# Kernel optimization log

Hardware: AMD Instinct MI355X
Metric: run time of the kernel (lower is better)

The kernel has to match this reference:

```python
import jax, jax.numpy as jnp
import numpy as np

NBINS = (128, 64, 32)   # knots per stacked transform
N_GENES = 5000
N_ELEM = 4_000_000


def _split_parameters(unnormalized):
    # mirror of QuadraticSplineStack._split_parameters: [heights(n), widths(n-1)] per transform
    splits = []
    for n in NBINS:
        splits += [n, n - 1]
    parts = jnp.split(unnormalized, np.cumsum(splits)[:-1].tolist(), axis=-1)
    return list(zip(parts[0::2], parts[1::2]))


def _bin_search(table, gix, x):
    # vectorized per-element binary search: searchsorted(table[gix], x, side='right') - 1,
    # clamped to valid bin range [0, K-2]. table: [G, K] sorted; gix, x: [N].
    K = table.shape[-1]
    lo = jnp.zeros(x.shape, jnp.int32)
    hi = jnp.full(x.shape, K, jnp.int32)
    for _ in range(int(np.ceil(np.log2(K + 1)))):
        mid = jnp.clip((lo + hi) // 2, 0, K - 1)
        pred = table[gix, mid] <= x
        lo = jnp.where(pred, mid + 1, lo)
        hi = jnp.where(pred, hi, mid)
    return jnp.clip(lo - 1, 0, K - 2)


def _quadratic_spline_forward(x, gix, unnorm_heights, unnorm_widths):
    # per-gene tables
    widths = jax.nn.softmax(unnorm_widths, axis=-1)                      # [G, n-1]
    locs = jnp.cumsum(widths, axis=-1)
    locs = jnp.pad(locs.at[:, -1].set(1.0), ((0, 0), (1, 0)))            # [G, n] bin_locations
    eh = jnp.exp(unnorm_heights)                                         # [G, n]
    area = jnp.sum(0.5 * (eh[:, :-1] + eh[:, 1:]) * widths, axis=-1, keepdims=True)
    heights = eh / area                                                  # pdf knot heights, integrates to 1
    cdf = jnp.cumsum(0.5 * (heights[:, :-1] + heights[:, 1:]) * widths, axis=-1)
    left_cdf = jnp.pad(cdf.at[:, -1].set(1.0), ((0, 0), (1, 0)))         # [G, n] bin_left_cdf

    # locate bin per element, then gather scalar coefficients
    b = _bin_search(locs, gix, x)                                        # [N] in [0, n-2]
    w = widths[gix, b]
    lh = heights[gix, b]
    rh = heights[gix, b + 1]
    bl = locs[gix, b]
    lc = left_cdf[gix, b]

    alpha = (x - bl) / w
    out = (0.5 * (rh - lh) * w) * alpha * alpha + (lh * w) * alpha + lc
    out = jnp.clip(out, 0.0, 1.0)
    logabsdet = jnp.log(alpha * (rh - lh) + lh)
    return out, logabsdet


def setup_inputs() -> dict:
    key = jax.random.key(0)
    k1, k2, k3 = jax.random.split(key, 3)
    x = jax.random.uniform(k1, (N_ELEM,), dtype=jnp.float32, minval=1e-4, maxval=1.0 - 1e-4)
    local_gene_ix = jax.random.randint(k2, (N_ELEM,), 0, N_GENES)
    total = sum(n + (n - 1) for n in NBINS)  # 445
    unnormalized = jax.random.normal(k3, (N_GENES, total), dtype=jnp.float32) * 0.1
    return {"x": x, "local_gene_ix": local_gene_ix, "unnormalized": unnormalized}


def reference(x, local_gene_ix, unnormalized):
    gix = local_gene_ix.astype(jnp.int32)
    outputs = x
    logabsdet = jnp.zeros_like(x)
    for uh, uw in _split_parameters(unnormalized):
        outputs, lad = _quadratic_spline_forward(outputs, gix, uh, uw)
        logabsdet = logabsdet + lad
    return outputs, logabsdet
```

## Files before the change

kernel.cpp:

```cpp
#include <hip/hip_runtime.h>
#include <hip/hip_bf16.h>
#include <hip/hip_fp16.h>

#define N_GENES_MAX 5000
#define PARAMS_PER_GENE 445

#define KNOTS_PER_GENE 224

__device__ uint2 g_knots[(size_t)N_GENES_MAX * KNOTS_PER_GENE];

static __device__ __forceinline__ unsigned short f2h(float f) {
    union { __half h; unsigned short u; } c;
    c.h = __float2half_rn(f);
    return c.u;
}
static __device__ __forceinline__ float h2f(unsigned short u) {
    union { unsigned short u; __half h; } c;
    c.u = u;
    return __half2float(c.h);
}

__global__ void build_knots(const float* __restrict__ params) {
    const int g = blockIdx.x;
    const int t = blockIdx.y;
    const int ns[3]   = {128, 64, 32};
    const int poff[3] = {0, 255, 382};
    const int koff[3] = {0, 128, 192};

    const int n = ns[t];
    const int m = n - 1;
    const float* ph = params + (size_t)g * PARAMS_PER_GENE + poff[t];
    const float* pw = ph + n;

    __shared__ float s_scan[128];
    __shared__ float s_h[129];
    __shared__ float s_red[128];
    __shared__ float s_loc[128];
    __shared__ float s_cdf[128];

    const int tid = threadIdx.x;

    float uw = (tid < m) ? pw[tid] : -1e30f;
    s_red[tid] = uw;
    __syncthreads();
    for (int s = 64; s > 0; s >>= 1) {
        if (tid < s) s_red[tid] = fmaxf(s_red[tid], s_red[tid + s]);
        __syncthreads();
    }
    const float mx = s_red[0];
    __syncthreads();
    float e = (tid < m) ? expf(uw - mx) : 0.0f;

    s_scan[tid] = e;
    __syncthreads();
    #pragma unroll
    for (int off = 1; off < 128; off <<= 1) {
        float v = (tid >= off) ? s_scan[tid - off] : 0.0f;
        __syncthreads();
        s_scan[tid] += v;
        __syncthreads();
    }
    const float S = s_scan[m - 1];
    const float invS = 1.0f / S;
    const float w_i = e * invS;
    if (tid == 0) s_loc[0] = 0.0f;
    if (tid < m) s_loc[tid + 1] = (tid == m - 1) ? 1.0f : s_scan[tid] * invS;
    __syncthreads();

    float uh = (tid < n) ? ph[tid] : 0.0f;
    float eh = (tid < n) ? expf(uh) : 0.0f;
    s_h[tid] = eh;
    if (tid == 0) s_h[128] = 0.0f;
    __syncthreads();
    float term = (tid < m) ? 0.5f * (s_h[tid] + s_h[tid + 1]) * w_i : 0.0f;
    s_red[tid] = term;
    __syncthreads();
    for (int s = 64; s > 0; s >>= 1) {
        if (tid < s) s_red[tid] += s_red[tid + s];
        __syncthreads();
    }
    const float area = s_red[0];
    __syncthreads();
    const float inv_area = 1.0f / area;
    const float hgt = eh * inv_area;

    float d = term * inv_area;
    s_scan[tid] = d;
    __syncthreads();
    #pragma unroll
    for (int off = 1; off < 128; off <<= 1) {
        float v = (tid >= off) ? s_scan[tid - off] : 0.0f;
        __syncthreads();
        s_scan[tid] += v;
        __syncthreads();
    }
    if (tid == 0) s_cdf[0] = 0.0f;
    if (tid < m) s_cdf[tid + 1] = (tid == m - 1) ? 1.0f : s_scan[tid];
    __syncthreads();

    if (tid < n) {
        uint2 kt;
        kt.x = __float_as_uint(s_loc[tid]);
        kt.y = ((unsigned)f2h(s_cdf[tid]) << 16) | (unsigned)f2h(hgt);
        g_knots[(size_t)g * KNOTS_PER_GENE + koff[t] + tid] = kt;
    }
}

template <int K>
__device__ __forceinline__ void spline_stage(const uint2* __restrict__ kn,
                                             float& x, float& lad) {
    int b = (int)(x * (float)(K - 1));
    b = (b < 0) ? 0 : ((b > K - 2) ? K - 2 : b);
    uint2 k0 = kn[b];
    uint2 k1 = kn[b + 1];
    float l0 = __uint_as_float(k0.x);
    float l1 = __uint_as_float(k1.x);
    while (b > 0 && l0 > x) {
        --b;
        k1 = k0; l1 = l0;
        k0 = kn[b]; l0 = __uint_as_float(k0.x);
    }
    while (b < K - 2 && l1 <= x) {
        ++b;
        k0 = k1; l0 = l1;
        k1 = kn[b + 1]; l1 = __uint_as_float(k1.x);
    }
    const float lh = h2f((unsigned short)(k0.y & 0xffffu));
    const float lc = h2f((unsigned short)(k0.y >> 16));
    const float rh = h2f((unsigned short)(k1.y & 0xffffu));
    const float w  = l1 - l0;
    const float alpha = (x - l0) / w;
    float o = (0.5f * (rh - lh) * w) * alpha * alpha + (lh * w) * alpha + lc;
    o = fminf(fmaxf(o, 0.0f), 1.0f);
    lad += __logf(alpha * (rh - lh) + lh);
    x = o;
}

__global__ void spline_eval_gather(const float* __restrict__ x_in,
                                   const int* __restrict__ gix,
                                   float* __restrict__ out, int N) {
    const int i = blockIdx.x * blockDim.x + threadIdx.x;
    if (i >= N) return;
    float x = x_in[i];
    const uint2* tab = g_knots + (size_t)gix[i] * KNOTS_PER_GENE;
    float lad = 0.0f;
    spline_stage<128>(tab, x, lad);
    spline_stage<64>(tab + 128, x, lad);
    spline_stage<32>(tab + 192, x, lad);
    out[i] = x;
    out[N + i] = lad;
}

extern "C" void kernel_launch(void* const* d_in, const int* in_sizes, int n_in,
                              void* d_out, int out_size, void* d_ws, size_t ws_size,
                              hipStream_t stream) {
    const float* x      = (const float*)d_in[0];
    const int*   gix    = (const int*)d_in[1];
    const float* params = (const float*)d_in[2];
    float* out = (float*)d_out;

    const int N = in_sizes[0];
    const int G = in_sizes[2] / PARAMS_PER_GENE;

    build_knots<<<dim3(G, 3), 128, 0, stream>>>(params);

    const int block = 256;
    spline_eval_gather<<<(N + block - 1) / block, block, 0, stream>>>(x, gix, out, N);
}
```

Baseline: 212.2 us.

## Store per-bin float4 records and process two elements per thread

Knot tables become per-bin float4 records holding left and right location, left CDF, and packed fp16 left and right heights. Each bin lookup is then a single 16-byte gather instead of two 8-byte gathers. The eval kernel also handles two elements per thread with vectorized float2/int2 loads and stores, giving more independent gathers in flight. The trade-off is a larger table footprint (16B per bin versus 8B per knot), which puts more pressure on L2/MALL for random per-gene access.

```diff
diff --git a/kernel.cpp b/kernel.cpp
--- a/kernel.cpp
+++ b/kernel.cpp
@@ -5,18 +5,18 @@
 #define N_GENES_MAX 5000
 #define PARAMS_PER_GENE 445
 
-#define KNOTS_PER_GENE 224
+__device__ float4 g_rec0[(size_t)N_GENES_MAX * 127];
+__device__ float4 g_rec1[(size_t)N_GENES_MAX * 63];
+__device__ float4 g_rec2[(size_t)N_GENES_MAX * 31];
 
-__device__ uint2 g_knots[(size_t)N_GENES_MAX * KNOTS_PER_GENE];
-
-static __device__ __forceinline__ unsigned short f2h(float f) {
+static __device__ __forceinline__ unsigned f2h(float f) {
     union { __half h; unsigned short u; } c;
     c.h = __float2half_rn(f);
-    return c.u;
+    return (unsigned)c.u;
 }
-static __device__ __forceinline__ float h2f(unsigned short u) {
+static __device__ __forceinline__ float h2f(unsigned u) {
     union { unsigned short u; __half h; } c;
-    c.u = u;
+    c.u = (unsigned short)u;
     return __half2float(c.h);
 }
 
@@ -25,7 +25,6 @@
     const int t = blockIdx.y;
     const int ns[3]   = {128, 64, 32};
     const int poff[3] = {0, 255, 382};
-    const int koff[3] = {0, 128, 192};
 
     const int n = ns[t];
     const int m = n - 1;
@@ -37,6 +36,7 @@
     __shared__ float s_red[128];
     __shared__ float s_loc[128];
     __shared__ float s_cdf[128];
+    __shared__ float s_hgt[128];
 
     const int tid = threadIdx.x;
 
@@ -62,9 +62,9 @@
     }
     const float S = s_scan[m - 1];
     const float invS = 1.0f / S;
-    const float w_i = e * invS;
     if (tid == 0) s_loc[0] = 0.0f;
     if (tid < m) s_loc[tid + 1] = (tid == m - 1) ? 1.0f : s_scan[tid] * invS;
+    const float w_i = e * invS;
     __syncthreads();
 
     float uh = (tid < n) ? ph[tid] : 0.0f;
@@ -82,7 +82,7 @@
     const float area = s_red[0];
     __syncthreads();
     const float inv_area = 1.0f / area;
-    const float hgt = eh * inv_area;
+    if (tid < n) s_hgt[tid] = eh * inv_area;
 
     float d = term * inv_area;
     s_scan[tid] = d;
@@ -98,57 +98,64 @@
     if (tid < m) s_cdf[tid + 1] = (tid == m - 1) ? 1.0f : s_scan[tid];
     __syncthreads();
 
-    if (tid < n) {
-        uint2 kt;
-        kt.x = __float_as_uint(s_loc[tid]);
-        kt.y = ((unsigned)f2h(s_cdf[tid]) << 16) | (unsigned)f2h(hgt);
-        g_knots[(size_t)g * KNOTS_PER_GENE + koff[t] + tid] = kt;
+    if (tid < m) {
+        float4 r;
+        r.x = s_loc[tid];
+        r.y = s_loc[tid + 1];
+        r.z = s_cdf[tid];
+        r.w = __uint_as_float((f2h(s_hgt[tid + 1]) << 16) | f2h(s_hgt[tid]));
+        if (t == 0)      g_rec0[(size_t)g * 127 + tid] = r;
+        else if (t == 1) g_rec1[(size_t)g * 63 + tid] = r;
+        else             g_rec2[(size_t)g * 31 + tid] = r;
     }
 }
 
 template <int K>
-__device__ __forceinline__ void spline_stage(const uint2* __restrict__ kn,
+static __device__ __forceinline__ void stage(const float4* __restrict__ rec,
                                              float& x, float& lad) {
     int b = (int)(x * (float)(K - 1));
     b = (b < 0) ? 0 : ((b > K - 2) ? K - 2 : b);
-    uint2 k0 = kn[b];
-    uint2 k1 = kn[b + 1];
-    float l0 = __uint_as_float(k0.x);
-    float l1 = __uint_as_float(k1.x);
-    while (b > 0 && l0 > x) {
-        --b;
-        k1 = k0; l1 = l0;
-        k0 = kn[b]; l0 = __uint_as_float(k0.x);
-    }
-    while (b < K - 2 && l1 <= x) {
-        ++b;
-        k0 = k1; l0 = l1;
-        k1 = kn[b + 1]; l1 = __uint_as_float(k1.x);
-    }
-    const float lh = h2f((unsigned short)(k0.y & 0xffffu));
-    const float lc = h2f((unsigned short)(k0.y >> 16));
-    const float rh = h2f((unsigned short)(k1.y & 0xffffu));
-    const float w  = l1 - l0;
-    const float alpha = (x - l0) / w;
-    float o = (0.5f * (rh - lh) * w) * alpha * alpha + (lh * w) * alpha + lc;
+    float4 r = rec[b];
+    while (b > 0 && r.x > x) { --b; r = rec[b]; }
+    while (b < K - 2 && r.y <= x) { ++b; r = rec[b]; }
+    const float w = r.y - r.x;
+    const float alpha = (x - r.x) / w;
+    const unsigned hp = __float_as_uint(r.w);
+    const float lh = h2f(hp & 0xffffu);
+    const float rh = h2f(hp >> 16);
+    float o = (0.5f * (rh - lh) * w) * alpha * alpha + (lh * w) * alpha + r.z;
     o = fminf(fmaxf(o, 0.0f), 1.0f);
     lad += __logf(alpha * (rh - lh) + lh);
     x = o;
 }
 
-__global__ void spline_eval_gather(const float* __restrict__ x_in,
-                                   const int* __restrict__ gix,
-                                   float* __restrict__ out, int N) {
+static __device__ __forceinline__ void eval_one(float& x, int g, float& lad) {
+    stage<128>(g_rec0 + (size_t)g * 127, x, lad);
+    stage<64> (g_rec1 + (size_t)g * 63,  x, lad);
+    stage<32> (g_rec2 + (size_t)g * 31,  x, lad);
+}
+
+__global__ void spline_eval(const float* __restrict__ x_in,
+                            const int* __restrict__ gix,
+                            float* __restrict__ out, int N) {
     const int i = blockIdx.x * blockDim.x + threadIdx.x;
-    if (i >= N) return;
-    float x = x_in[i];
-    const uint2* tab = g_knots + (size_t)gix[i] * KNOTS_PER_GENE;
-    float lad = 0.0f;
-    spline_stage<128>(tab, x, lad);
-    spline_stage<64>(tab + 128, x, lad);
-    spline_stage<32>(tab + 192, x, lad);
-    out[i] = x;
-    out[N + i] = lad;
+    const int i2 = i * 2;
+    if (i2 + 1 < N) {
+        const float2 xv = *(const float2*)(x_in + i2);
+        const int2   gv = *(const int2*)(gix + i2);
+        float x0 = xv.x, x1 = xv.y;
+        float l0 = 0.0f, l1 = 0.0f;
+        eval_one(x0, gv.x, l0);
+        eval_one(x1, gv.y, l1);
+        *(float2*)(out + i2)     = make_float2(x0, x1);
+        *(float2*)(out + N + i2) = make_float2(l0, l1);
+    } else if (i2 < N) {
+        float x0 = x_in[i2];
+        float l0 = 0.0f;
+        eval_one(x0, gix[i2], l0);
+        out[i2] = x0;
+        out[N + i2] = l0;
+    }
 }
 
 extern "C" void kernel_launch(void* const* d_in, const int* in_sizes, int n_in,
@@ -165,5 +172,6 @@
     build_knots<<<dim3(G, 3), 128, 0, stream>>>(params);
 
     const int block = 256;
-    spline_eval_gather<<<(N + block - 1) / block, block, 0, stream>>>(x, gix, out, N);
+    const int nh = (N + 1) / 2;
+    spline_eval<<<(nh + block - 1) / block, block, 0, stream>>>(x, gix, out, N);
 }
```

Measured after the change: 483.7 us. 128% more time.
